# Kernel optimization log

Measured on AMD Instinct MI355X. Metric: run time of the kernel, lower is better.

## Reference

```python
import jax, jax.numpy as jnp
import numpy as np

N_M, N_D, N_A = 100000, 30000, 80000


def setup_inputs() -> dict:
    key = jax.random.key(0)
    ks = jax.random.split(key, 24)
    d_in, d_h, d_out = 64, 64, 32
    inp = {
        "x_movie": jax.random.normal(ks[0], (N_M, d_in), jnp.float32),
        "x_director": jax.random.normal(ks[1], (N_D, d_in), jnp.float32),
        "x_actor": jax.random.normal(ks[2], (N_A, d_in), jnp.float32),
        "src_md": jax.random.randint(ks[3], (1500000,), 0, N_M, jnp.int32),
        "dst_md": jax.random.randint(ks[4], (1500000,), 0, N_D, jnp.int32),
        "ew_md": jax.random.uniform(ks[5], (1500000,), jnp.float32),
        "src_dm": jax.random.randint(ks[6], (1500000,), 0, N_D, jnp.int32),
        "dst_dm": jax.random.randint(ks[7], (1500000,), 0, N_M, jnp.int32),
        "ew_dm": jax.random.uniform(ks[8], (1500000,), jnp.float32),
        "src_ma": jax.random.randint(ks[9], (2000000,), 0, N_M, jnp.int32),
        "dst_ma": jax.random.randint(ks[10], (2000000,), 0, N_A, jnp.int32),
        "ew_ma": jax.random.uniform(ks[11], (2000000,), jnp.float32),
        "src_am": jax.random.randint(ks[12], (2000000,), 0, N_A, jnp.int32),
        "dst_am": jax.random.randint(ks[13], (2000000,), 0, N_M, jnp.int32),
        "ew_am": jax.random.uniform(ks[14], (2000000,), jnp.float32),
        "W1_rel": jax.random.normal(ks[15], (4, d_in, d_h), jnp.float32) * 0.05,
        "b1": jax.random.normal(ks[16], (4, d_h), jnp.float32) * 0.05,
        "W1_root": jax.random.normal(ks[17], (4, d_in, d_h), jnp.float32) * 0.05,
        "W2_rel": jax.random.normal(ks[18], (4, d_h, d_out), jnp.float32) * 0.05,
        "b2": jax.random.normal(ks[19], (4, d_out), jnp.float32) * 0.05,
        "W2_root": jax.random.normal(ks[20], (4, d_h, d_out), jnp.float32) * 0.05,
    }
    return inp


def _hetero_layer(x_m, x_d, x_a, edges, ews, W_rel, b, W_root):
    # relation order: 0 = movie->director, 1 = director->movie,
    #                 2 = movie->actor,    3 = actor->movie
    (src_md, dst_md, src_dm, dst_dm, src_ma, dst_ma, src_am, dst_am) = edges
    (ew_md, ew_dm, ew_ma, ew_am) = ews
    # GraphConv: aggregate edge-weighted source features, then linear.
    agg_md = jax.ops.segment_sum(x_m[src_md] * ew_md[:, None], dst_md, num_segments=N_D)
    agg_dm = jax.ops.segment_sum(x_d[src_dm] * ew_dm[:, None], dst_dm, num_segments=N_M)
    agg_ma = jax.ops.segment_sum(x_m[src_ma] * ew_ma[:, None], dst_ma, num_segments=N_A)
    agg_am = jax.ops.segment_sum(x_a[src_am] * ew_am[:, None], dst_am, num_segments=N_M)
    out_d = agg_md @ W_rel[0] + b[0] + x_d @ W_root[0]
    out_m = (agg_dm @ W_rel[1] + b[1] + x_m @ W_root[1]) \
          + (agg_am @ W_rel[3] + b[3] + x_m @ W_root[3])  # HeteroConv aggr='sum'
    out_a = agg_ma @ W_rel[2] + b[2] + x_a @ W_root[2]
    return out_m, out_d, out_a


def reference(x_movie, x_director, x_actor,
              src_md, dst_md, ew_md, src_dm, dst_dm, ew_dm,
              src_ma, dst_ma, ew_ma, src_am, dst_am, ew_am,
              W1_rel, b1, W1_root, W2_rel, b2, W2_root):
    edges = (src_md, dst_md, src_dm, dst_dm, src_ma, dst_ma, src_am, dst_am)
    ews = (ew_md, ew_dm, ew_ma, ew_am)
    h_m, h_d, h_a = _hetero_layer(x_movie, x_director, x_actor, edges, ews, W1_rel, b1, W1_root)
    h_m, h_d, h_a = jax.nn.relu(h_m), jax.nn.relu(h_d), jax.nn.relu(h_a)
    o_m, o_d, o_a = _hetero_layer(h_m, h_d, h_a, edges, ews, W2_rel, b2, W2_root)
    return o_m, o_d, o_a
```

## Files before the change

kernel.cpp:

```cpp
#include <hip/hip_runtime.h>

#define N_M 100000
#define N_D 30000
#define N_A 80000

#define CSHIFT 14
#define NC_M 7
#define NC_D 2
#define NC_A 5

#define BO_MD 0
#define BO_DM (BO_MD + N_D * NC_M)
#define BO_MA (BO_DM + N_M * NC_D)
#define BO_AM (BO_MA + N_A * NC_M)
#define B_TOT (BO_AM + N_M * NC_A)

#define FBITS 12
#define NFINE 4096
#define NBUCK ((B_TOT + NFINE - 1) / NFINE)
#define T_A 4096

typedef unsigned int u32;
typedef unsigned short u16;
typedef unsigned long long u64;

__device__ __forceinline__ u16 f2bf(float f) {
  u32 u = __float_as_uint(f);
  return (u16)((u + 0x7FFFu + ((u >> 16) & 1u)) >> 16);
}
__device__ __forceinline__ float bf2f(u16 b) {
  return __uint_as_float(((u32)b) << 16);
}
__device__ __forceinline__ float bf2f_hi(u32 v) {
  return __uint_as_float(v & 0xFFFF0000u);
}
__device__ __forceinline__ u32 pack_edge(int src, float ew) {
  return ((u32)src << 15) | ((u32)f2bf(ew) & 0x7FFFu);
}

struct Rel { const int* src; const int* dst; const float* ew; int nE; int binBase; int nC; };
struct Rel4 { Rel r[4]; int blkStart[5]; };

__global__ __launch_bounds__(256) void phase0(Rel4 P, int* __restrict__ bucketHist) {
  __shared__ u32 lh[512];
  int tid = threadIdx.x;
  int b = blockIdx.x, s = 0;
  while (b >= P.blkStart[s + 1]) s++;
  const Rel R = P.r[s];
  int base = (b - P.blkStart[s]) * T_A;
  for (int i = tid; i < 512; i += 256) lh[i] = 0;
  __syncthreads();
#pragma unroll 4
  for (int k = 0; k < 16; k++) {
    int e = base + tid + k * 256;
    if (e < R.nE) {
      int key = R.binBase + R.dst[e] * R.nC + (R.src[e] >> CSHIFT);
      atomicAdd(&lh[key >> FBITS], 1u);
    }
  }
  __syncthreads();
  for (int i = tid; i < 512; i += 256) if (lh[i]) atomicAdd(&bucketHist[i], (int)lh[i]);
}

__global__ __launch_bounds__(256) void scan_bucket(const int* __restrict__ bucketHist,
                                                   int* __restrict__ bucketBase,
                                                   int* __restrict__ cursor) {
  __shared__ int wsum[4];
  int tid = threadIdx.x;
  int j0 = tid * 2;
  int a0 = (j0 < NBUCK) ? bucketHist[j0] : 0;
  int a1 = (j0 + 1 < NBUCK) ? bucketHist[j0 + 1] : 0;
  int ssum = a0 + a1;
  int lane = tid & 63, wid = tid >> 6;
  int sc = ssum;
#pragma unroll
  for (int off = 1; off < 64; off <<= 1) { int t = __shfl_up(sc, off, 64); if (lane >= off) sc += t; }
  if (lane == 63) wsum[wid] = sc;
  __syncthreads();
  int wex = 0, tot = 0;
  for (int w = 0; w < 4; w++) { int t = wsum[w]; if (w < wid) wex += t; tot += t; }
  int ex = wex + sc - ssum;
  if (j0 < NBUCK) { bucketBase[j0] = ex; cursor[j0] = ex; }
  if (j0 + 1 < NBUCK) { bucketBase[j0 + 1] = ex + a0; cursor[j0 + 1] = ex + a0; }
  if (tid == 0) bucketBase[NBUCK] = tot;
}

__global__ __launch_bounds__(256) void phaseA(Rel4 P, int* __restrict__ cursor,
                                              u64* __restrict__ tmp) {
  __shared__ u32 hist[512], lstart[512], cur[512], gbase[512];
  __shared__ u64 stage[T_A];
  __shared__ u32 wsum[4];
  int tid = threadIdx.x;
  int b = blockIdx.x, s = 0;
  while (b >= P.blkStart[s + 1]) s++;
  const Rel R = P.r[s];
  int base = (b - P.blkStart[s]) * T_A;
  int valid = min(T_A, R.nE - base);
  for (int i = tid; i < 512; i += 256) hist[i] = 0;
  __syncthreads();
#pragma unroll 4
  for (int k = 0; k < 16; k++) {
    int e = base + tid + k * 256;
    if (e < R.nE) {
      int key = R.binBase + R.dst[e] * R.nC + (R.src[e] >> CSHIFT);
      atomicAdd(&hist[key >> FBITS], 1u);
    }
  }
  __syncthreads();
  int c0 = tid * 2;
  u32 h0 = hist[c0], h1 = hist[c0 + 1];
  u32 ssum = h0 + h1;
  int lane = tid & 63, wid = tid >> 6;
  u32 sc = ssum;
#pragma unroll
  for (int off = 1; off < 64; off <<= 1) { int t = __shfl_up((int)sc, off, 64); if (lane >= off) sc += (u32)t; }
  if (lane == 63) wsum[wid] = sc;
  __syncthreads();
  u32 wex = 0;
  for (int w = 0; w < 4; w++) if (w < wid) wex += wsum[w];
  u32 ex = wex + sc - ssum;
  lstart[c0] = ex;       cur[c0] = ex;
  lstart[c0 + 1] = ex + h0; cur[c0 + 1] = ex + h0;
  if (h0) gbase[c0] = (u32)atomicAdd(&cursor[c0], (int)h0);
  if (h1) gbase[c0 + 1] = (u32)atomicAdd(&cursor[c0 + 1], (int)h1);
  __syncthreads();
#pragma unroll 4
  for (int k = 0; k < 16; k++) {
    int e = base + tid + k * 256;
    if (e < R.nE) {
      int srcv = R.src[e];
      int key = R.binBase + R.dst[e] * R.nC + (srcv >> CSHIFT);
      u32 slot = atomicAdd(&cur[key >> FBITS], 1u);
      stage[slot] = ((u64)(u32)key << 32) | pack_edge(srcv, R.ew[e]);
    }
  }
  __syncthreads();
  for (int i = tid; i < valid; i += 256) {
    u64 v = stage[i];
    u32 c = (u32)(v >> (32 + FBITS));
    tmp[gbase[c] + ((u32)i - lstart[c])] = v;
  }
}

__global__ __launch_bounds__(256) void phaseB(const u64* __restrict__ tmp,
                                              const int* __restrict__ bucketBase,
                                              u32* __restrict__ pairs,
                                              int* __restrict__ bins) {
  __shared__ u32 h2[NFINE], cur2[NFINE];
  __shared__ u32 wsum[4];
  int c = blockIdx.x, tid = threadIdx.x;
  int s0 = bucketBase[c], s1 = bucketBase[c + 1];
  for (int i = tid; i < NFINE; i += 256) h2[i] = 0;
  __syncthreads();
  for (int e = s0 + tid; e < s1; e += 256) {
    u32 fine = (u32)(tmp[e] >> 32) & (NFINE - 1);
    atomicAdd(&h2[fine], 1u);
  }
  __syncthreads();
  int f0 = tid * 16;
  u32 v[16], ssum = 0;
#pragma unroll
  for (int i = 0; i < 16; i++) { v[i] = h2[f0 + i]; ssum += v[i]; }
  int lane = tid & 63, wid = tid >> 6;
  u32 sc = ssum;
#pragma unroll
  for (int off = 1; off < 64; off <<= 1) { int t = __shfl_up((int)sc, off, 64); if (lane >= off) sc += (u32)t; }
  if (lane == 63) wsum[wid] = sc;
  __syncthreads();
  u32 wex = 0;
  for (int w = 0; w < 4; w++) if (w < wid) wex += wsum[w];
  u32 ex = wex + sc - ssum;
  int binBase0 = c << FBITS;
#pragma unroll
  for (int i = 0; i < 16; i++) {
    int gb = binBase0 + f0 + i;
    if (gb < B_TOT) bins[gb] = s0 + (int)ex;
    cur2[f0 + i] = ex;
    ex += v[i];
  }
  if (c == NBUCK - 1 && tid == 0) bins[B_TOT] = s1;
  __syncthreads();
  for (int e = s0 + tid; e < s1; e += 256) {
    u64 t = tmp[e];
    u32 fine = (u32)(t >> 32) & (NFINE - 1);
    u32 pos = atomicAdd(&cur2[fine], 1u);
    pairs[s0 + pos] = (u32)t;
  }
}

__global__ __launch_bounds__(256) void l1_tr_m(
    const float* __restrict__ x,
    const float* __restrict__ Wr0, const float* __restrict__ Wr2,
    const float* __restrict__ Wt1, const float* __restrict__ Wt3,
    const float* __restrict__ b1a, const float* __restrict__ b1b,
    u16* __restrict__ t0, u16* __restrict__ t2, u16* __restrict__ r, int n) {
  __shared__ float A[4096], B[4096], C[4096];
  for (int i = threadIdx.x * 4; i < 4096; i += 1024) {
    *(float4*)&A[i] = *(const float4*)&Wr0[i];
    *(float4*)&B[i] = *(const float4*)&Wr2[i];
    float4 p = *(const float4*)&Wt1[i], q = *(const float4*)&Wt3[i];
    *(float4*)&C[i] = make_float4(p.x + q.x, p.y + q.y, p.z + q.z, p.w + q.w);
  }
  __syncthreads();
  int lane = threadIdx.x & 63, wid = threadIdx.x >> 6;
  int wave = blockIdx.x * 4 + wid, nW = gridDim.x * 4;
  float bj = b1a[lane] + b1b[lane];
  for (int base = wave * 4; base < n; base += nW * 4) {
    int n0 = base, n1 = min(base + 1, n - 1), n2 = min(base + 2, n - 1), n3 = min(base + 3, n - 1);
    float o0a = 0, o0b = 0, o0c = bj, o1a = 0, o1b = 0, o1c = bj;
    float o2a = 0, o2b = 0, o2c = bj, o3a = 0, o3b = 0, o3c = bj;
#pragma unroll 4
    for (int k = 0; k < 64; k++) {
      float wa = A[k * 64 + lane], wb = B[k * 64 + lane], wc = C[k * 64 + lane];
      float x0 = x[(size_t)n0 * 64 + k], x1 = x[(size_t)n1 * 64 + k];
      float x2 = x[(size_t)n2 * 64 + k], x3 = x[(size_t)n3 * 64 + k];
      o0a = fmaf(x0, wa, o0a); o0b = fmaf(x0, wb, o0b); o0c = fmaf(x0, wc, o0c);
      o1a = fmaf(x1, wa, o1a); o1b = fmaf(x1, wb, o1b); o1c = fmaf(x1, wc, o1c);
      o2a = fmaf(x2, wa, o2a); o2b = fmaf(x2, wb, o2b); o2c = fmaf(x2, wc, o2c);
      o3a = fmaf(x3, wa, o3a); o3b = fmaf(x3, wb, o3b); o3c = fmaf(x3, wc, o3c);
    }
    t0[(size_t)n0 * 64 + lane] = f2bf(o0a); t2[(size_t)n0 * 64 + lane] = f2bf(o0b); r[(size_t)n0 * 64 + lane] = f2bf(o0c);
    if (base + 1 < n) { t0[(size_t)n1 * 64 + lane] = f2bf(o1a); t2[(size_t)n1 * 64 + lane] = f2bf(o1b); r[(size_t)n1 * 64 + lane] = f2bf(o1c); }
    if (base + 2 < n) { t0[(size_t)n2 * 64 + lane] = f2bf(o2a); t2[(size_t)n2 * 64 + lane] = f2bf(o2b); r[(size_t)n2 * 64 + lane] = f2bf(o2c); }
    if (base + 3 < n) { t0[(size_t)n3 * 64 + lane] = f2bf(o3a); t2[(size_t)n3 * 64 + lane] = f2bf(o3b); r[(size_t)n3 * 64 + lane] = f2bf(o3c); }
  }
}

__global__ __launch_bounds__(256) void l1_tr_s2(
    const float* __restrict__ x1, const float* __restrict__ Wrel1,
    const float* __restrict__ Wroot1, const float* __restrict__ bias1,
    u16* __restrict__ t1o, u16* __restrict__ r1o, int n1, int nBlk1,
    const float* __restrict__ x2, const float* __restrict__ Wrel2,
    const float* __restrict__ Wroot2, const float* __restrict__ bias2,
    u16* __restrict__ t2o, u16* __restrict__ r2o, int n2) {
  __shared__ float A[4096], C[4096];
  bool first = (int)blockIdx.x < nBlk1;
  const float* x = first ? x1 : x2;
  const float* Wrel = first ? Wrel1 : Wrel2;
  const float* Wroot = first ? Wroot1 : Wroot2;
  const float* bias = first ? bias1 : bias2;
  u16* t = first ? t1o : t2o;
  u16* r = first ? r1o : r2o;
  int n = first ? n1 : n2;
  int blk = first ? blockIdx.x : blockIdx.x - nBlk1;
  int nBlk = first ? nBlk1 : (gridDim.x - nBlk1);
  for (int i = threadIdx.x * 4; i < 4096; i += 1024) {
    *(float4*)&A[i] = *(const float4*)&Wrel[i];
    *(float4*)&C[i] = *(const float4*)&Wroot[i];
  }
  __syncthreads();
  int lane = threadIdx.x & 63, wid = threadIdx.x >> 6;
  int wave = blk * 4 + wid, nW = nBlk * 4;
  float bj = bias[lane];
  for (int base = wave * 4; base < n; base += nW * 4) {
    int n0 = base, n1_ = min(base + 1, n - 1), n2_ = min(base + 2, n - 1), n3_ = min(base + 3, n - 1);
    float o0a = 0, o0c = bj, o1a = 0, o1c = bj, o2a = 0, o2c = bj, o3a = 0, o3c = bj;
#pragma unroll 4
    for (int k = 0; k < 64; k++) {
      float wa = A[k * 64 + lane], wc = C[k * 64 + lane];
      float x0 = x[(size_t)n0 * 64 + k], xx1 = x[(size_t)n1_ * 64 + k];
      float xx2 = x[(size_t)n2_ * 64 + k], xx3 = x[(size_t)n3_ * 64 + k];
      o0a = fmaf(x0, wa, o0a); o0c = fmaf(x0, wc, o0c);
      o1a = fmaf(xx1, wa, o1a); o1c = fmaf(xx1, wc, o1c);
      o2a = fmaf(xx2, wa, o2a); o2c = fmaf(xx2, wc, o2c);
      o3a = fmaf(xx3, wa, o3a); o3c = fmaf(xx3, wc, o3c);
    }
    t[(size_t)n0 * 64 + lane] = f2bf(o0a); r[(size_t)n0 * 64 + lane] = f2bf(o0c);
    if (base + 1 < n) { t[(size_t)n1_ * 64 + lane] = f2bf(o1a); r[(size_t)n1_ * 64 + lane] = f2bf(o1c); }
    if (base + 2 < n) { t[(size_t)n2_ * 64 + lane] = f2bf(o2a); r[(size_t)n2_ * 64 + lane] = f2bf(o2c); }
    if (base + 3 < n) { t[(size_t)n3_ * 64 + lane] = f2bf(o3a); r[(size_t)n3_ * 64 + lane] = f2bf(o3c); }
  }
}

__device__ __forceinline__ void g2_pair(u32 pa, u32 pb,
    const u16* __restrict__ tbl, u32 lanebyte, u32 hm,
    float& a0, float& a1) {
  u32 offa = (pa >> 15) << 7, offd = ((pb >> 15) << 7) - offa;
  u32 wa = (pa & 0x7FFFu) << 16, wd = ((pb & 0x7FFFu) << 16) ^ wa;
  u32 v = *(const u32*)((const char*)tbl + ((hm & offd) + offa + lanebyte));
  float w = __uint_as_float((hm & wd) ^ wa);
  a0 = fmaf(w, bf2f((u16)v), a0);
  a1 = fmaf(w, bf2f_hi(v), a1);
}

__device__ __forceinline__ void g2y_pair(u32 pa, u32 pb,
    const u16* __restrict__ tbl, const u16* __restrict__ ytbl,
    u32 lanebyte, u32 ylanebyte, u32 hm,
    float& a0, float& a1, float& ay) {
  u32 ra = pa >> 15, rb = pb >> 15;
  u32 offa = ra << 7, offd = (rb << 7) - offa;
  u32 yoa = ra << 6,  yod = (rb << 6) - yoa;
  u32 wa = (pa & 0x7FFFu) << 16, wd = ((pb & 0x7FFFu) << 16) ^ wa;
  u32 v = *(const u32*)((const char*)tbl + ((hm & offd) + offa + lanebyte));
  u16 q = *(const u16*)((const char*)ytbl + ((hm & yod) + yoa + ylanebyte));
  float w = __uint_as_float((hm & wd) ^ wa);
  a0 = fmaf(w, bf2f((u16)v), a0);
  a1 = fmaf(w, bf2f_hi(v), a1);
  ay = fmaf(w, bf2f(q), ay);
}

#define RL(x, i) ((u32)__builtin_amdgcn_readlane((int)(x), (i)))

__device__ __forceinline__ void gather2_seg64(
    int s0, int s1, const u32* __restrict__ pairs,
    const u16* __restrict__ tbl, u32 lanebyte, u32 hm, int lane, u32 pw0,
    float& a0, float& a1) {
  int base = s0;
  u32 pw = pw0;
  for (;;) {
    int cnt = s1 - base; if (cnt > 64) cnt = 64;
    int e = 0;
    for (; e + 8 <= cnt; e += 8) {
      u32 p0 = RL(pw, e),     p1 = RL(pw, e + 1), p2 = RL(pw, e + 2), p3 = RL(pw, e + 3);
      u32 p4 = RL(pw, e + 4), p5 = RL(pw, e + 5), p6 = RL(pw, e + 6), p7 = RL(pw, e + 7);
      g2_pair(p0, p1, tbl, lanebyte, hm, a0, a1);
      g2_pair(p2, p3, tbl, lanebyte, hm, a0, a1);
      g2_pair(p4, p5, tbl, lanebyte, hm, a0, a1);
      g2_pair(p6, p7, tbl, lanebyte, hm, a0, a1);
    }
    if (e + 4 <= cnt) {
      u32 p0 = RL(pw, e), p1 = RL(pw, e + 1), p2 = RL(pw, e + 2), p3 = RL(pw, e + 3);
      g2_pair(p0, p1, tbl, lanebyte, hm, a0, a1);
      g2_pair(p2, p3, tbl, lanebyte, hm, a0, a1);
      e += 4;
    }
    if (e + 2 <= cnt) {
      u32 p0 = RL(pw, e), p1 = RL(pw, e + 1);
      g2_pair(p0, p1, tbl, lanebyte, hm, a0, a1);
      e += 2;
    }
    if (e < cnt) {
      u32 p = RL(pw, e);
      g2_pair(p, p & 0xFFFF8000u, tbl, lanebyte, hm, a0, a1);
    }
    base += 64;
    if (base >= s1) break;
    pw = (base + lane < s1) ? pairs[base + lane] : 0u;
  }
}

__device__ __forceinline__ void gather2y_seg64(
    int s0, int s1, const u32* __restrict__ pairs,
    const u16* __restrict__ tbl, const u16* __restrict__ ytbl,
    u32 lanebyte, u32 ylanebyte, u32 hm, int lane, u32 pw0,
    float& a0, float& a1, float& ay) {
  int base = s0;
  u32 pw = pw0;
  for (;;) {
    int cnt = s1 - base; if (cnt > 64) cnt = 64;
    int e = 0;
    for (; e + 8 <= cnt; e += 8) {
      u32 p0 = RL(pw, e),     p1 = RL(pw, e + 1), p2 = RL(pw, e + 2), p3 = RL(pw, e + 3);
      u32 p4 = RL(pw, e + 4), p5 = RL(pw, e + 5), p6 = RL(pw, e + 6), p7 = RL(pw, e + 7);
      g2y_pair(p0, p1, tbl, ytbl, lanebyte, ylanebyte, hm, a0, a1, ay);
      g2y_pair(p2, p3, tbl, ytbl, lanebyte, ylanebyte, hm, a0, a1, ay);
      g2y_pair(p4, p5, tbl, ytbl, lanebyte, ylanebyte, hm, a0, a1, ay);
      g2y_pair(p6, p7, tbl, ytbl, lanebyte, ylanebyte, hm, a0, a1, ay);
    }
    if (e + 4 <= cnt) {
      u32 p0 = RL(pw, e), p1 = RL(pw, e + 1), p2 = RL(pw, e + 2), p3 = RL(pw, e + 3);
      g2y_pair(p0, p1, tbl, ytbl, lanebyte, ylanebyte, hm, a0, a1, ay);
      g2y_pair(p2, p3, tbl, ytbl, lanebyte, ylanebyte, hm, a0, a1, ay);
      e += 4;
    }
    if (e + 2 <= cnt) {
      u32 p0 = RL(pw, e), p1 = RL(pw, e + 1);
      g2y_pair(p0, p1, tbl, ytbl, lanebyte, ylanebyte, hm, a0, a1, ay);
      e += 2;
    }
    if (e < cnt) {
      u32 p = RL(pw, e);
      g2y_pair(p, p & 0xFFFF8000u, tbl, ytbl, lanebyte, ylanebyte, hm, a0, a1, ay);
    }
    base += 64;
    if (base >= s1) break;
    pw = (base + lane < s1) ? pairs[base + lane] : 0u;
  }
}

__device__ __forceinline__ void gathero_32(
    int s0, int s1, const u32* __restrict__ pairs,
    const u16* __restrict__ ytbl, int lanebyte, int oaddr, int lane,
    float& a0, float& a1, float& a2, float& a3) {
  for (int base = s0; base < s1; base += 64) {
    u32 pw = 0;
    if (base + lane < s1) pw = pairs[base + lane];
    int ng = min(s1 - base, 64);
    ng = (ng + 7) >> 3;
#pragma unroll 2
    for (int g = 0; g < ng; g++) {
      u32 p = (u32)__builtin_amdgcn_ds_bpermute(oaddr + (g << 5), (int)pw);
      u32 off = ((p >> 15) << 6) + lanebyte;
      float w = __uint_as_float((p & 0x7FFFu) << 16);
      uint2 v = *(const uint2*)((const char*)ytbl + off);
      a0 = fmaf(w, bf2f((u16)v.x), a0);
      a1 = fmaf(w, bf2f_hi(v.x), a1);
      a2 = fmaf(w, bf2f((u16)v.y), a2);
      a3 = fmaf(w, bf2f_hi(v.y), a3);
    }
  }
}

struct F1Side {
  const u16 *tbl, *ytbl, *r1;
  const float *W2r, *W2t, *b2;
  u16 *y; float *out;
  int n, nC, binBase;
};

__global__ __launch_bounds__(512) void fused1(
    const int* __restrict__ bins, const u32* __restrict__ pairs,
    F1Side D, F1Side A, int nBlkD) {
  __shared__ float Wy[2048], Wt[2048];
  __shared__ float bs[32];
  __shared__ __align__(16) float scr[8][64];
  bool isD = (int)blockIdx.x < nBlkD;
  F1Side S = isD ? D : A;
  int blk = isD ? blockIdx.x : blockIdx.x - nBlkD;
  for (int i = threadIdx.x; i < 2048; i += 512) { Wy[i] = S.W2r[i]; Wt[i] = S.W2t[i]; }
  if (threadIdx.x < 32) bs[threadIdx.x] = S.b2[threadIdx.x];
  __syncthreads();
  int lane = threadIdx.x & 63, wid = threadIdx.x >> 6;
  int j = lane & 31, half = lane >> 5;
  u32 lanebyte = (u32)j << 2;
  u32 ylanebyte = (u32)j << 1;
  u32 hm = half ? 0xFFFFFFFFu : 0u;
  int node0 = (blk * 8 + wid) * 8;
  int bnd = bins[S.binBase + (node0 + min(lane, 8)) * S.nC];
  float acc0[8], acc1[8], accy[8];
#pragma unroll
  for (int i = 0; i < 8; i++) { acc0[i] = 0.f; acc1[i] = 0.f; accy[i] = 0.f; }
  u32 pwp[8];
#pragma unroll
  for (int i = 0; i < 8; i++) {
    int s0 = __builtin_amdgcn_readlane(bnd, i);
    int s1 = __builtin_amdgcn_readlane(bnd, i + 1);
    pwp[i] = (node0 + i < S.n && s0 + lane < s1) ? pairs[s0 + lane] : 0u;
  }
#pragma unroll
  for (int i = 0; i < 8; i++) {
    int s0 = __builtin_amdgcn_readlane(bnd, i);
    int s1 = __builtin_amdgcn_readlane(bnd, i + 1);
    if (node0 + i < S.n)
      gather2y_seg64(s0, s1, pairs, S.tbl, S.ytbl, lanebyte, ylanebyte, hm, lane, pwp[i],
                     acc0[i], acc1[i], accy[i]);
  }
#pragma unroll
  for (int i = 0; i < 8; i++) {
    int node = node0 + i;
    if (node >= S.n) continue;
    float a0 = acc0[i] + __shfl_xor(acc0[i], 32);
    float a1 = acc1[i] + __shfl_xor(acc1[i], 32);
    float ayt = accy[i] + __shfl_xor(accy[i], 32);
    u32 rv = *(const u32*)&S.r1[(size_t)node * 64 + 2 * j];
    float hv0 = fmaxf(a0 + bf2f((u16)rv), 0.f);
    float hv1 = fmaxf(a1 + bf2f_hi(rv), 0.f);
    if (!half) *(float2*)&scr[wid][2 * j] = make_float2(hv0, hv1);
    float oy = 0.f, ot = 0.f;
#pragma unroll
    for (int kk = 0; kk < 32; kk++) {
      int k = (half << 5) + kk;
      float s = scr[wid][k];
      oy = fmaf(s, Wy[k * 32 + j], oy);
      ot = fmaf(s, Wt[k * 32 + j], ot);
    }
    oy += __shfl_xor(oy, 32);
    ot += __shfl_xor(ot, 32);
    if (lane < 32) {
      S.y[(size_t)node * 32 + lane] = f2bf(oy);
      S.out[(size_t)node * 32 + lane] = ot + bs[lane] + ayt;
    }
  }
}

__global__ __launch_bounds__(512) void fusedm(
    const int* __restrict__ bins, const u32* __restrict__ pairs,
    const u16* __restrict__ tbl1,
    const u16* __restrict__ tbl2,
    const u16* __restrict__ r1,
    const float* __restrict__ W2r0, const float* __restrict__ W2r2,
    const float* __restrict__ W2t1, const float* __restrict__ W2t3,
    const float* __restrict__ b2a, const float* __restrict__ b2b,
    u16* __restrict__ y0, u16* __restrict__ y2, float* __restrict__ oroot, int n) {
  __shared__ float Wy0[2048], Wy2[2048], Wt[2048];
  __shared__ float bs[32];
  __shared__ __align__(16) float scr[8][64];
  for (int i = threadIdx.x; i < 2048; i += 512) {
    Wy0[i] = W2r0[i]; Wy2[i] = W2r2[i]; Wt[i] = W2t1[i] + W2t3[i];
  }
  if (threadIdx.x < 32) bs[threadIdx.x] = b2a[threadIdx.x] + b2b[threadIdx.x];
  __syncthreads();
  int lane = threadIdx.x & 63, wid = threadIdx.x >> 6;
  int j = lane & 31, half = lane >> 5;
  u32 lanebyte = (u32)j << 2;
  u32 hm = half ? 0xFFFFFFFFu : 0u;
  int node0 = (blockIdx.x * 8 + wid) * 8;
  int bdm = bins[BO_DM + (node0 + min(lane, 8)) * NC_D];
  int bam = bins[BO_AM + (node0 + min(lane, 8)) * NC_A];
  float acc0[8], acc1[8];
#pragma unroll
  for (int i = 0; i < 8; i++) { acc0[i] = 0.f; acc1[i] = 0.f; }
  {
    u32 pwp[8];
#pragma unroll
    for (int i = 0; i < 8; i++) {
      int s0 = __builtin_amdgcn_readlane(bdm, i);
      int s1 = __builtin_amdgcn_readlane(bdm, i + 1);
      pwp[i] = (node0 + i < n && s0 + lane < s1) ? pairs[s0 + lane] : 0u;
    }
#pragma unroll
    for (int i = 0; i < 8; i++) {
      int s0 = __builtin_amdgcn_readlane(bdm, i);
      int s1 = __builtin_amdgcn_readlane(bdm, i + 1);
      if (node0 + i < n)
        gather2_seg64(s0, s1, pairs, tbl1, lanebyte, hm, lane, pwp[i], acc0[i], acc1[i]);
    }
  }
  {
    u32 pwp[8];
#pragma unroll
    for (int i = 0; i < 8; i++) {
      int s0 = __builtin_amdgcn_readlane(bam, i);
      int s1 = __builtin_amdgcn_readlane(bam, i + 1);
      pwp[i] = (node0 + i < n && s0 + lane < s1) ? pairs[s0 + lane] : 0u;
    }
#pragma unroll
    for (int i = 0; i < 8; i++) {
      int s0 = __builtin_amdgcn_readlane(bam, i);
      int s1 = __builtin_amdgcn_readlane(bam, i + 1);
      if (node0 + i < n)
        gather2_seg64(s0, s1, pairs, tbl2, lanebyte, hm, lane, pwp[i], acc0[i], acc1[i]);
    }
  }
#pragma unroll
  for (int i = 0; i < 8; i++) {
    int node = node0 + i;
    if (node >= n) continue;
    float a0 = acc0[i] + __shfl_xor(acc0[i], 32);
    float a1 = acc1[i] + __shfl_xor(acc1[i], 32);
    u32 rv = *(const u32*)&r1[(size_t)node * 64 + 2 * j];
    float hv0 = fmaxf(a0 + bf2f((u16)rv), 0.f);
    float hv1 = fmaxf(a1 + bf2f_hi(rv), 0.f);
    if (!half) *(float2*)&scr[wid][2 * j] = make_float2(hv0, hv1);
    float o0 = 0.f, o2 = 0.f, ot = 0.f;
#pragma unroll
    for (int kk = 0; kk < 32; kk++) {
      int k = (half << 5) + kk;
      float s = scr[wid][k];
      o0 = fmaf(s, Wy0[k * 32 + j], o0);
      o2 = fmaf(s, Wy2[k * 32 + j], o2);
      ot = fmaf(s, Wt[k * 32 + j], ot);
    }
    o0 += __shfl_xor(o0, 32);
    o2 += __shfl_xor(o2, 32);
    ot += __shfl_xor(ot, 32);
    if (lane < 32) {
      y0[(size_t)node * 32 + lane] = f2bf(o0);
      y2[(size_t)node * 32 + lane] = f2bf(o2);
      oroot[(size_t)node * 32 + lane] = ot + bs[lane];
    }
  }
}

__global__ __launch_bounds__(256) void outm(
    const int* __restrict__ bins, const u32* __restrict__ pairs,
    const u16* __restrict__ y1,
    const u16* __restrict__ y2,
    float* __restrict__ out, int n) {
  int lane = threadIdx.x & 63, wid = threadIdx.x >> 6;
  int node0 = (blockIdx.x * 4 + wid) * 8;
  int j8 = lane & 7;
  int lanebyte = j8 << 3;
  int oaddr = (lane >> 3) << 2;
  int bdm = bins[BO_DM + (node0 + min(lane, 8)) * NC_D];
  int bam = bins[BO_AM + (node0 + min(lane, 8)) * NC_A];
  float acc0[8], acc1[8], acc2[8], acc3[8];
#pragma unroll
  for (int i = 0; i < 8; i++) { acc0[i] = 0.f; acc1[i] = 0.f; acc2[i] = 0.f; acc3[i] = 0.f; }
#pragma unroll
  for (int i = 0; i < 8; i++) {
    int s0 = __builtin_amdgcn_readlane(bdm, i);
    int s1 = __builtin_amdgcn_readlane(bdm, i + 1);
    if (node0 + i < n) gathero_32(s0, s1, pairs, y1, lanebyte, oaddr, lane,
                                  acc0[i], acc1[i], acc2[i], acc3[i]);
  }
#pragma unroll
  for (int i = 0; i < 8; i++) {
    int s0 = __builtin_amdgcn_readlane(bam, i);
    int s1 = __builtin_amdgcn_readlane(bam, i + 1);
    if (node0 + i < n) gathero_32(s0, s1, pairs, y2, lanebyte, oaddr, lane,
                                  acc0[i], acc1[i], acc2[i], acc3[i]);
  }
#pragma unroll
  for (int i = 0; i < 8; i++) {
    int node = node0 + i;
    if (node >= n) continue;
    float a0 = acc0[i], a1 = acc1[i], a2 = acc2[i], a3 = acc3[i];
    a0 += __shfl_xor(a0, 8); a0 += __shfl_xor(a0, 16); a0 += __shfl_xor(a0, 32);
    a1 += __shfl_xor(a1, 8); a1 += __shfl_xor(a1, 16); a1 += __shfl_xor(a1, 32);
    a2 += __shfl_xor(a2, 8); a2 += __shfl_xor(a2, 16); a2 += __shfl_xor(a2, 32);
    a3 += __shfl_xor(a3, 8); a3 += __shfl_xor(a3, 16); a3 += __shfl_xor(a3, 32);
    if (lane < 8) {
      float4* o = (float4*)((char*)out + (size_t)node * 128 + (j8 << 4));
      float4 v = *o;
      v.x += a0; v.y += a1; v.z += a2; v.w += a3;
      *o = v;
    }
  }
}

static inline int nblkA(long long e) { return (int)((e + T_A - 1) / T_A); }

extern "C" void kernel_launch(void* const* d_in, const int* in_sizes, int n_in,
                              void* d_out, int out_size, void* d_ws, size_t ws_size,
                              hipStream_t stream) {
  const float* x_m = (const float*)d_in[0];
  const float* x_d = (const float*)d_in[1];
  const float* x_a = (const float*)d_in[2];
  const int* src_md = (const int*)d_in[3];
  const int* dst_md = (const int*)d_in[4];
  const float* ew_md = (const float*)d_in[5];
  const int* src_dm = (const int*)d_in[6];
  const int* dst_dm = (const int*)d_in[7];
  const float* ew_dm = (const float*)d_in[8];
  const int* src_ma = (const int*)d_in[9];
  const int* dst_ma = (const int*)d_in[10];
  const float* ew_ma = (const float*)d_in[11];
  const int* src_am = (const int*)d_in[12];
  const int* dst_am = (const int*)d_in[13];
  const float* ew_am = (const float*)d_in[14];
  const float* W1_rel = (const float*)d_in[15];
  const float* b1 = (const float*)d_in[16];
  const float* W1_root = (const float*)d_in[17];
  const float* W2_rel = (const float*)d_in[18];
  const float* b2 = (const float*)d_in[19];
  const float* W2_root = (const float*)d_in[20];

  const int E_md = in_sizes[3];
  const int E_dm = in_sizes[6];
  const int E_ma = in_sizes[9];
  const int E_am = in_sizes[12];
  const long long E_tot = (long long)E_md + E_dm + E_ma + E_am;

  char* w = (char*)d_ws;
  u64* tmp = (u64*)w;       w += (size_t)E_tot * 8;
  u32* pairs = (u32*)w;     w += (size_t)E_tot * 4;
  int* bins = (int*)w;      w += (size_t)(B_TOT + 1) * 4;
  int* bucketHist = (int*)w; w += 512 * 4;
  int* bucketBase = (int*)w; w += (NBUCK + 1) * 4;
  int* cursor = (int*)w;     w += 512 * 4;
  u16* r_d  = (u16*)w;      w += (size_t)N_D * 64 * 2;
  u16* r_a  = (u16*)w;      w += (size_t)N_A * 64 * 2;
  u16* y_md = (u16*)w;      w += (size_t)N_M * 32 * 2;
  u16* y_dm = (u16*)w;      w += (size_t)N_D * 32 * 2;
  u16* y_ma = (u16*)w;      w += (size_t)N_M * 32 * 2;
  u16* y_am = (u16*)w;      w += (size_t)N_A * 32 * 2;
  if ((size_t)(w - (char*)d_ws) > ws_size) return;
  char* ta = (char*)tmp;
  u16* t_md = (u16*)ta;     ta += (size_t)N_M * 64 * 2;
  u16* t_dm = (u16*)ta;     ta += (size_t)N_D * 64 * 2;
  u16* t_ma = (u16*)ta;     ta += (size_t)N_M * 64 * 2;
  u16* t_am = (u16*)ta;     ta += (size_t)N_A * 64 * 2;
  u16* r_m  = (u16*)ta;     ta += (size_t)N_M * 64 * 2;

  float* o_m = (float*)d_out;
  float* o_d = o_m + (size_t)N_M * 32;
  float* o_a = o_d + (size_t)N_D * 32;

  hipMemsetAsync(bucketHist, 0, 512 * 4, stream);

  Rel4 P;
  P.r[0] = { src_md, dst_md, ew_md, E_md, BO_MD, NC_M };
  P.r[1] = { src_dm, dst_dm, ew_dm, E_dm, BO_DM, NC_D };
  P.r[2] = { src_ma, dst_ma, ew_ma, E_ma, BO_MA, NC_M };
  P.r[3] = { src_am, dst_am, ew_am, E_am, BO_AM, NC_A };
  P.blkStart[0] = 0;
  P.blkStart[1] = P.blkStart[0] + nblkA(E_md);
  P.blkStart[2] = P.blkStart[1] + nblkA(E_dm);
  P.blkStart[3] = P.blkStart[2] + nblkA(E_ma);
  P.blkStart[4] = P.blkStart[3] + nblkA(E_am);

  phase0<<<P.blkStart[4], 256, 0, stream>>>(P, bucketHist);
  scan_bucket<<<1, 256, 0, stream>>>(bucketHist, bucketBase, cursor);
  phaseA<<<P.blkStart[4], 256, 0, stream>>>(P, cursor, tmp);
  phaseB<<<NBUCK, 256, 0, stream>>>(tmp, bucketBase, pairs, bins);

  l1_tr_m<<<768, 256, 0, stream>>>(x_m, W1_rel + 0 * 4096, W1_rel + 2 * 4096,
                                   W1_root + 1 * 4096, W1_root + 3 * 4096,
                                   b1 + 1 * 64, b1 + 3 * 64, t_md, t_ma, r_m, N_M);
  l1_tr_s2<<<1024, 256, 0, stream>>>(
      x_d, W1_rel + 1 * 4096, W1_root + 0 * 4096, b1 + 0 * 64, t_dm, r_d, N_D, 512,
      x_a, W1_rel + 3 * 4096, W1_root + 2 * 4096, b1 + 2 * 64, t_am, r_a, N_A);

  fusedm<<<(N_M + 63) / 64, 512, 0, stream>>>(bins, pairs, t_dm, t_am, r_m,
      W2_rel + 0 * 2048, W2_rel + 2 * 2048, W2_root + 1 * 2048, W2_root + 3 * 2048,
      b2 + 1 * 32, b2 + 3 * 32, y_md, y_ma, o_m, N_M);

  int nBlkD = (N_D + 63) / 64;
  int nBlkA_ = (N_A + 63) / 64;
  F1Side Dside = { t_md, y_md, r_d, W2_rel + 1 * 2048, W2_root + 0 * 2048, b2 + 0 * 32,
                   y_dm, o_d, N_D, NC_M, BO_MD };
  F1Side Aside = { t_ma, y_ma, r_a, W2_rel + 3 * 2048, W2_root + 2 * 2048, b2 + 2 * 32,
                   y_am, o_a, N_A, NC_M, BO_MA };
  fused1<<<nBlkD + nBlkA_, 512, 0, stream>>>(bins, pairs, Dside, Aside, nBlkD);

  outm<<<(N_M + 31) / 32, 256, 0, stream>>>(bins, pairs, y_dm, y_am, o_m, N_M);
}
```

Baseline: 875.2 us.

## Gather per source chunk across nodes and split fused1 into per-side launches

The fused1 and fusedm gathers now loop over source-index chunks. Each wave visits the edges of all 8 of its nodes that fall in one chunk before moving to the next, instead of walking each node's full edge list in one go. The aim is to keep concurrent table reads inside one ~16K-row slice so they hit cache better. The cost is more, shorter segments with extra readlane, branch and padding overhead, since each node's few edges are now split seven or five ways. fused1 is also split into separate director and actor launches with plain arguments, and bin index reads are clamped to stay in range.

Result: slower. 964.8 us (+10.2%).

```diff
diff --git a/kernel.cpp b/kernel.cpp
--- a/kernel.cpp
+++ b/kernel.cpp
@@ -401,58 +401,56 @@
   }
 }
 
-struct F1Side {
-  const u16 *tbl, *ytbl, *r1;
-  const float *W2r, *W2t, *b2;
-  u16 *y; float *out;
-  int n, nC, binBase;
-};
-
 __global__ __launch_bounds__(512) void fused1(
     const int* __restrict__ bins, const u32* __restrict__ pairs,
-    F1Side D, F1Side A, int nBlkD) {
+    const u16* __restrict__ tbl, const u16* __restrict__ ytbl,
+    const u16* __restrict__ r1,
+    const float* __restrict__ W2r, const float* __restrict__ W2t,
+    const float* __restrict__ b2s,
+    u16* __restrict__ y, float* __restrict__ out,
+    int n, int binBase) {
   __shared__ float Wy[2048], Wt[2048];
   __shared__ float bs[32];
   __shared__ __align__(16) float scr[8][64];
-  bool isD = (int)blockIdx.x < nBlkD;
-  F1Side S = isD ? D : A;
-  int blk = isD ? blockIdx.x : blockIdx.x - nBlkD;
-  for (int i = threadIdx.x; i < 2048; i += 512) { Wy[i] = S.W2r[i]; Wt[i] = S.W2t[i]; }
-  if (threadIdx.x < 32) bs[threadIdx.x] = S.b2[threadIdx.x];
+  for (int i = threadIdx.x; i < 2048; i += 512) { Wy[i] = W2r[i]; Wt[i] = W2t[i]; }
+  if (threadIdx.x < 32) bs[threadIdx.x] = b2s[threadIdx.x];
   __syncthreads();
   int lane = threadIdx.x & 63, wid = threadIdx.x >> 6;
   int j = lane & 31, half = lane >> 5;
   u32 lanebyte = (u32)j << 2;
   u32 ylanebyte = (u32)j << 1;
   u32 hm = half ? 0xFFFFFFFFu : 0u;
-  int node0 = (blk * 8 + wid) * 8;
-  int bnd = bins[S.binBase + (node0 + min(lane, 8)) * S.nC];
+  int node0 = (blockIdx.x * 8 + wid) * 8;
+  int bidx = min(node0 * NC_M + min(lane, 8 * NC_M), n * NC_M);
+  int bnd = bins[binBase + bidx];
   float acc0[8], acc1[8], accy[8];
 #pragma unroll
   for (int i = 0; i < 8; i++) { acc0[i] = 0.f; acc1[i] = 0.f; accy[i] = 0.f; }
-  u32 pwp[8];
-#pragma unroll
-  for (int i = 0; i < 8; i++) {
-    int s0 = __builtin_amdgcn_readlane(bnd, i);
-    int s1 = __builtin_amdgcn_readlane(bnd, i + 1);
-    pwp[i] = (node0 + i < S.n && s0 + lane < s1) ? pairs[s0 + lane] : 0u;
-  }
-#pragma unroll
-  for (int i = 0; i < 8; i++) {
-    int s0 = __builtin_amdgcn_readlane(bnd, i);
-    int s1 = __builtin_amdgcn_readlane(bnd, i + 1);
-    if (node0 + i < S.n)
-      gather2y_seg64(s0, s1, pairs, S.tbl, S.ytbl, lanebyte, ylanebyte, hm, lane, pwp[i],
-                     acc0[i], acc1[i], accy[i]);
+  for (int c = 0; c < NC_M; c++) {
+    u32 pwp[8];
+#pragma unroll
+    for (int i = 0; i < 8; i++) {
+      int s0 = __builtin_amdgcn_readlane(bnd, i * NC_M + c);
+      int s1 = __builtin_amdgcn_readlane(bnd, i * NC_M + c + 1);
+      pwp[i] = (node0 + i < n && s0 + lane < s1) ? pairs[s0 + lane] : 0u;
+    }
+#pragma unroll
+    for (int i = 0; i < 8; i++) {
+      int s0 = __builtin_amdgcn_readlane(bnd, i * NC_M + c);
+      int s1 = __builtin_amdgcn_readlane(bnd, i * NC_M + c + 1);
+      if (node0 + i < n && s0 < s1)
+        gather2y_seg64(s0, s1, pairs, tbl, ytbl, lanebyte, ylanebyte, hm, lane, pwp[i],
+                       acc0[i], acc1[i], accy[i]);
+    }
   }
 #pragma unroll
   for (int i = 0; i < 8; i++) {
     int node = node0 + i;
-    if (node >= S.n) continue;
+    if (node >= n) continue;
     float a0 = acc0[i] + __shfl_xor(acc0[i], 32);
     float a1 = acc1[i] + __shfl_xor(acc1[i], 32);
     float ayt = accy[i] + __shfl_xor(accy[i], 32);
-    u32 rv = *(const u32*)&S.r1[(size_t)node * 64 + 2 * j];
+    u32 rv = *(const u32*)&r1[(size_t)node * 64 + 2 * j];
     float hv0 = fmaxf(a0 + bf2f((u16)rv), 0.f);
     float hv1 = fmaxf(a1 + bf2f_hi(rv), 0.f);
     if (!half) *(float2*)&scr[wid][2 * j] = make_float2(hv0, hv1);
@@ -467,8 +465,8 @@
     oy += __shfl_xor(oy, 32);
     ot += __shfl_xor(ot, 32);
     if (lane < 32) {
-      S.y[(size_t)node * 32 + lane] = f2bf(oy);
-      S.out[(size_t)node * 32 + lane] = ot + bs[lane] + ayt;
+      y[(size_t)node * 32 + lane] = f2bf(oy);
+      out[(size_t)node * 32 + lane] = ot + bs[lane] + ayt;
     }
   }
 }
@@ -495,8 +493,9 @@
   u32 lanebyte = (u32)j << 2;
   u32 hm = half ? 0xFFFFFFFFu : 0u;
   int node0 = (blockIdx.x * 8 + wid) * 8;
-  int bdm = bins[BO_DM + (node0 + min(lane, 8)) * NC_D];
-  int bam = bins[BO_AM + (node0 + min(lane, 8)) * NC_A];
+  int bdm = bins[BO_DM + min(node0 + min(lane, 8), n) * NC_D];
+  int baidx = min(node0 * NC_A + min(lane, 8 * NC_A), n * NC_A);
+  int bam = bins[BO_AM + baidx];
   float acc0[8], acc1[8];
 #pragma unroll
   for (int i = 0; i < 8; i++) { acc0[i] = 0.f; acc1[i] = 0.f; }
@@ -512,23 +511,23 @@
     for (int i = 0; i < 8; i++) {
       int s0 = __builtin_amdgcn_readlane(bdm, i);
       int s1 = __builtin_amdgcn_readlane(bdm, i + 1);
-      if (node0 + i < n)
+      if (node0 + i < n && s0 < s1)
         gather2_seg64(s0, s1, pairs, tbl1, lanebyte, hm, lane, pwp[i], acc0[i], acc1[i]);
     }
   }
-  {
+  for (int c = 0; c < NC_A; c++) {
     u32 pwp[8];
 #pragma unroll
     for (int i = 0; i < 8; i++) {
-      int s0 = __builtin_amdgcn_readlane(bam, i);
-      int s1 = __builtin_amdgcn_readlane(bam, i + 1);
+      int s0 = __builtin_amdgcn_readlane(bam, i * NC_A + c);
+      int s1 = __builtin_amdgcn_readlane(bam, i * NC_A + c + 1);
       pwp[i] = (node0 + i < n && s0 + lane < s1) ? pairs[s0 + lane] : 0u;
     }
 #pragma unroll
     for (int i = 0; i < 8; i++) {
-      int s0 = __builtin_amdgcn_readlane(bam, i);
-      int s1 = __builtin_amdgcn_readlane(bam, i + 1);
-      if (node0 + i < n)
+      int s0 = __builtin_amdgcn_readlane(bam, i * NC_A + c);
+      int s1 = __builtin_amdgcn_readlane(bam, i * NC_A + c + 1);
+      if (node0 + i < n && s0 < s1)
         gather2_seg64(s0, s1, pairs, tbl2, lanebyte, hm, lane, pwp[i], acc0[i], acc1[i]);
     }
   }
@@ -572,8 +571,8 @@
   int j8 = lane & 7;
   int lanebyte = j8 << 3;
   int oaddr = (lane >> 3) << 2;
-  int bdm = bins[BO_DM + (node0 + min(lane, 8)) * NC_D];
-  int bam = bins[BO_AM + (node0 + min(lane, 8)) * NC_A];
+  int bdm = bins[BO_DM + min(node0 + min(lane, 8), n) * NC_D];
+  int bam = bins[BO_AM + min(node0 + min(lane, 8), n) * NC_A];
   float acc0[8], acc1[8], acc2[8], acc3[8];
 #pragma unroll
   for (int i = 0; i < 8; i++) { acc0[i] = 0.f; acc1[i] = 0.f; acc2[i] = 0.f; acc3[i] = 0.f; }
@@ -696,13 +695,10 @@
       W2_rel + 0 * 2048, W2_rel + 2 * 2048, W2_root + 1 * 2048, W2_root + 3 * 2048,
       b2 + 1 * 32, b2 + 3 * 32, y_md, y_ma, o_m, N_M);
 
-  int nBlkD = (N_D + 63) / 64;
-  int nBlkA_ = (N_A + 63) / 64;
-  F1Side Dside = { t_md, y_md, r_d, W2_rel + 1 * 2048, W2_root + 0 * 2048, b2 + 0 * 32,
-                   y_dm, o_d, N_D, NC_M, BO_MD };
-  F1Side Aside = { t_ma, y_ma, r_a, W2_rel + 3 * 2048, W2_root + 2 * 2048, b2 + 2 * 32,
-                   y_am, o_a, N_A, NC_M, BO_MA };
-  fused1<<<nBlkD + nBlkA_, 512, 0, stream>>>(bins, pairs, Dside, Aside, nBlkD);
+  fused1<<<(N_D + 63) / 64, 512, 0, stream>>>(bins, pairs, t_md, y_md, r_d,
+      W2_rel + 1 * 2048, W2_root + 0 * 2048, b2 + 0 * 32, y_dm, o_d, N_D, BO_MD);
+  fused1<<<(N_A + 63) / 64, 512, 0, stream>>>(bins, pairs, t_ma, y_ma, r_a,
+      W2_rel + 3 * 2048, W2_root + 2 * 2048, b2 + 2 * 32, y_am, o_a, N_A, BO_MA);
 
   outm<<<(N_M + 31) / 32, 256, 0, stream>>>(bins, pairs, y_dm, y_am, o_m, N_M);
 }
```
